# Kernel tuning notes

Measured on AMD Instinct MI355X. Metric: run time of the kernel, lower is better.

The kernel has to match this reference:

```python
import jax, jax.numpy as jnp
import numpy as np

NUM_ROUNDS = 64
D_HIDDEN = 256
B = 16384

# MD5 message schedule g(i)
_SCHED = np.array([i if i < 16 else ((5*i+1) % 16 if i < 32 else ((3*i+5) % 16 if i < 48 else (7*i) % 16)) for i in range(64)], dtype=np.int32)
# MD5 per-round shift amounts
_SHIFT = np.array([7,12,17,22]*4 + [5,9,14,20]*4 + [4,11,16,23]*4 + [6,10,15,21]*4, dtype=np.float32)
# round_info[i] = [i/64, shift[i]/25], shape (64, 2)
_ROUND_INFO = np.stack([np.arange(64, dtype=np.float32) / 64.0, _SHIFT / 25.0], axis=-1)


def setup_inputs() -> dict:
    key = jax.random.key(0)
    ks = jax.random.split(key, 8)
    return {
        "message_bytes": jax.random.uniform(ks[0], (B, 64), dtype=jnp.float32),
        "initial_state": jax.random.uniform(ks[1], (B, 16), dtype=jnp.float32),
        "W1": jax.random.normal(ks[2], (NUM_ROUNDS, 22, D_HIDDEN), dtype=jnp.float32) * (1.0 / np.sqrt(22.0)),
        "b1": jax.random.normal(ks[3], (NUM_ROUNDS, D_HIDDEN), dtype=jnp.float32) * 0.02,
        "W2": jax.random.normal(ks[4], (NUM_ROUNDS, D_HIDDEN, D_HIDDEN), dtype=jnp.float32) * (1.0 / np.sqrt(float(D_HIDDEN))),
        "b2": jax.random.normal(ks[5], (NUM_ROUNDS, D_HIDDEN), dtype=jnp.float32) * 0.02,
        "W3": jax.random.normal(ks[6], (NUM_ROUNDS, D_HIDDEN, 16), dtype=jnp.float32) * (1.0 / np.sqrt(float(D_HIDDEN))),
        "b3": jax.random.normal(ks[7], (NUM_ROUNDS, 16), dtype=jnp.float32) * 0.02,
    }


def reference(message_bytes, initial_state, W1, b1, W2, b2, W3, b3):
    Bsz = message_bytes.shape[0]
    msg_words = message_bytes.reshape(Bsz, 16, 4)
    # pre-gather the scheduled word per round: (64, B, 4)
    words = jnp.transpose(msg_words[:, jnp.asarray(_SCHED), :], (1, 0, 2))
    round_info = jnp.asarray(_ROUND_INFO)  # (64, 2)

    def step(state, xs):
        word, rinfo, w1, c1, w2, c2, w3, c3 = xs
        x = jnp.concatenate([state, word, jnp.broadcast_to(rinfo, (state.shape[0], 2))], axis=-1)  # (B, 22)
        h = jax.nn.gelu(x @ w1 + c1, approximate=False)
        h = jax.nn.gelu(h @ w2 + c2, approximate=False)
        return h @ w3 + c3, None

    final_state, _ = jax.lax.scan(step, initial_state, (words, round_info, W1, b1, W2, b2, W3, b3))
    return final_state
```

## Files before the change

kernel.cpp:

```cpp
#include <hip/hip_runtime.h>
#include <stdint.h>


using bf16x8   = __attribute__((ext_vector_type(8))) __bf16;
using floatx4  = __attribute__((ext_vector_type(4))) float;
using ushort4v = __attribute__((ext_vector_type(4))) unsigned short;

__constant__ int c_sched[64] = {
  0,1,2,3,4,5,6,7,8,9,10,11,12,13,14,15,
  1,6,11,0,5,10,15,4,9,14,3,8,13,2,7,12,
  5,8,11,14,1,4,7,10,13,0,3,6,9,12,15,2,
  0,7,14,5,12,3,10,1,8,15,6,13,4,11,2,9
};
__constant__ float c_shift[64] = {
  7,12,17,22,7,12,17,22,7,12,17,22,7,12,17,22,
  5,9,14,20,5,9,14,20,5,9,14,20,5,9,14,20,
  4,11,16,23,4,11,16,23,4,11,16,23,4,11,16,23,
  6,10,15,21,6,10,15,21,6,10,15,21,6,10,15,21
};

__device__ __forceinline__ unsigned short bfbits(__bf16 b) {
  union { __bf16 b; unsigned short u; } v; v.b = b; return v.u;
}
__device__ __forceinline__ float gelu_f(float x) {
  float ax = fabsf(x);
  float t  = __builtin_amdgcn_rcpf(__builtin_fmaf(0.33270222f, ax, 1.0f));
  float e  = __builtin_amdgcn_exp2f(x * x * -0.72134752f);
  float poly = t * __builtin_fmaf(t, __builtin_fmaf(t, 0.7478556f, -0.0958798f),
                                  0.3480242f);
  float er = __builtin_fmaf(-poly, e, 1.0f);
  er = copysignf(er, x);
  float hx = 0.5f * x;
  return __builtin_fmaf(hx, er, hx);
}
__device__ __forceinline__ floatx4 mfma16(bf16x8 a, bf16x8 b, floatx4 c) {
  return __builtin_amdgcn_mfma_f32_16x16x32_bf16(a, b, c, 0, 0, 0);
}
struct BfPair { unsigned short h, l; };
__device__ __forceinline__ BfPair split2(float s) {
  __bf16 hb = (__bf16)s;
  __bf16 lb = (__bf16)(s - (float)hb);
  BfPair p; p.h = bfbits(hb); p.l = bfbits(lb); return p;
}

#define N1G (64*16*64)
#define N2G (64*16*8*64)
#define N3G (64*8*64)

__global__ void pack_w(const float* __restrict__ W1,
                       const float* __restrict__ W2,
                       const float* __restrict__ W3,
                       unsigned short* __restrict__ P) {
  int gid = blockIdx.x * blockDim.x + threadIdx.x;
  if (gid >= N1G + N2G + N3G) return;
  unsigned short v[8];
  unsigned short* dst;
  if (gid < N1G) {
    int lane = gid & 63, t = (gid >> 6) & 15, r = gid >> 10;
    int qq = lane >> 4, mm = lane & 15;
    #pragma unroll
    for (int j = 0; j < 8; ++j) {
      int k = 8*qq + j;
      v[j] = (k < 22) ? bfbits((__bf16)W1[(r*22 + k)*256 + 16*t + mm]) : (unsigned short)0;
    }
    dst = P + (size_t)gid * 8;
  } else if (gid < N1G + N2G) {
    int g = gid - N1G;
    int lane = g & 63, c = (g >> 6) & 7, t = (g >> 9) & 15, r = g >> 13;
    int qq = lane >> 4, mm = lane & 15;
    #pragma unroll
    for (int j = 0; j < 8; ++j) {
      int k = 32*c + 8*qq + j;
      v[j] = bfbits((__bf16)W2[((size_t)r*256 + k)*256 + 16*t + mm]);
    }
    dst = P + (size_t)(N1G + g) * 8;
  } else {
    int g = gid - N1G - N2G;
    int lane = g & 63, c = (g >> 6) & 7, r = g >> 9;
    int qq = lane >> 4, mm = lane & 15;
    #pragma unroll
    for (int j = 0; j < 8; ++j) {
      int k = 32*c + 8*qq + j;
      v[j] = bfbits((__bf16)W3[(r*256 + k)*16 + mm]);
    }
    dst = P + (size_t)(N1G + N2G + g) * 8;
  }
  ushort4v lo = { v[0],v[1],v[2],v[3] }, hi = { v[4],v[5],v[6],v[7] };
  *(ushort4v*)dst = lo;
  *(ushort4v*)(dst + 4) = hi;
}

#define NG  2
#define SXW 36
#define SH 264
#define SM 66

__global__ __launch_bounds__(256, 2) void md5_main(
    const float* __restrict__ msg,
    const float* __restrict__ st0,
    const float* __restrict__ b1,
    const float* __restrict__ b2,
    const float* __restrict__ b3,
    const unsigned short* __restrict__ P,
    float* __restrict__ out)
{
  __shared__ unsigned short xh[4][NG][16][SXW], xl[4][NG][16][SXW];
  __shared__ unsigned short hA[NG][16][SH], hB[NG][16][SH];
  __shared__ unsigned short msgb[NG*16][SM], msgl[NG*16][SM];

  const int tid  = threadIdx.x;
  const int wv   = tid >> 6;
  const int lane = tid & 63;
  const int q    = lane >> 4;
  const int ln   = lane & 15;
  const int row0 = blockIdx.x * (NG*16);

  const unsigned short* P1 = P;
  const unsigned short* P2 = P + (size_t)N1G * 8;
  const unsigned short* P3 = P + (size_t)(N1G + N2G) * 8;

  for (int i = lane; i < NG*16*SXW; i += 64) {
    (&xh[wv][0][0][0])[i] = 0; (&xl[wv][0][0][0])[i] = 0;
  }
  {
    int idx = tid * 8, rr = idx >> 6, cc = idx & 63;
    floatx4 v0 = *(const floatx4*)(msg + (size_t)(row0 + rr)*64 + cc);
    floatx4 v1 = *(const floatx4*)(msg + (size_t)(row0 + rr)*64 + cc + 4);
    #pragma unroll
    for (int j = 0; j < 4; ++j) {
      BfPair p0 = split2(v0[j]);
      BfPair p1 = split2(v1[j]);
      msgb[rr][cc + j]     = p0.h;  msgl[rr][cc + j]     = p0.l;
      msgb[rr][cc + 4 + j] = p1.h;  msgl[rr][cc + 4 + j] = p1.l;
    }
  }
  #pragma unroll
  for (int g = 0; g < NG; ++g) {
    floatx4 v = *(const floatx4*)(st0 + (size_t)(row0 + g*16 + ln)*16 + 4*q);
    ushort4v h4, l4;
    #pragma unroll
    for (int e = 0; e < 4; ++e) { BfPair p = split2(v[e]); h4[e] = p.h; l4[e] = p.l; }
    *(ushort4v*)&xh[wv][g][ln][4*q] = h4;
    *(ushort4v*)&xl[wv][g][ln][4*q] = l4;
  }
  __syncthreads();
  if (lane < NG*16) {
    int g = lane >> 4, n = lane & 15, rrow = lane;
    int s = c_sched[0];
    BfPair i1p = split2(c_shift[0] / 25.0f);
    #pragma unroll
    for (int j = 0; j < 4; ++j) {
      xh[wv][g][n][16+j] = msgb[rrow][4*s+j];
      xl[wv][g][n][16+j] = msgl[rrow][4*s+j];
    }
    xh[wv][g][n][20] = 0;     xl[wv][g][n][20] = 0;
    xh[wv][g][n][21] = i1p.h; xl[wv][g][n][21] = i1p.l;
  }

  #pragma unroll 1
  for (int r = 0; r < 64; ++r) {
    floatx4 bb1[4];
    bf16x8  a1[4];
    const unsigned short* p1 = P1 + ((size_t)(r*16 + 4*wv)*64 + lane)*8;
    #pragma unroll
    for (int tt = 0; tt < 4; ++tt) {
      a1[tt]  = *(const bf16x8*)(p1 + (size_t)tt*512);
      bb1[tt] = *(const floatx4*)(b1 + r*256 + (4*wv + tt)*16 + 4*q);
    }
    bf16x8 bxh[NG], bxl[NG];
    #pragma unroll
    for (int g = 0; g < NG; ++g) {
      bxh[g] = *(const bf16x8*)&xh[wv][g][ln][8*q];
      bxl[g] = *(const bf16x8*)&xl[wv][g][ln][8*q];
    }
    #pragma unroll
    for (int tt = 0; tt < 4; ++tt) {
      int f0 = (4*wv + tt)*16 + 4*q;
      #pragma unroll
      for (int g = 0; g < NG; ++g) {
        floatx4 acc = bb1[tt];
        acc = mfma16(a1[tt], bxl[g], acc);
        acc = mfma16(a1[tt], bxh[g], acc);
        ushort4v h4;
        #pragma unroll
        for (int e = 0; e < 4; ++e) h4[e] = bfbits((__bf16)gelu_f(acc[e]));
        *(ushort4v*)&hA[g][ln][f0] = h4;
      }
    }
    __syncthreads();

    bf16x8 a3[8];
    {
      const unsigned short* p3 = P3 + ((size_t)(r*8)*64 + lane)*8;
      #pragma unroll
      for (int c = 0; c < 8; ++c) a3[c] = *(const bf16x8*)(p3 + (size_t)c*512);
    }
    floatx4 bb3 = *(const floatx4*)(b3 + r*16 + 4*q);
    floatx4 bb2[4];
    #pragma unroll
    for (int tt = 0; tt < 4; ++tt)
      bb2[tt] = *(const floatx4*)(b2 + r*256 + (4*wv + tt)*16 + 4*q);

    bf16x8 Bf[NG][8];
    #pragma unroll
    for (int g = 0; g < NG; ++g)
      #pragma unroll
      for (int c = 0; c < 8; ++c) Bf[g][c] = *(const bf16x8*)&hA[g][ln][32*c + 8*q];

    const unsigned short* p2 = P2 + ((size_t)((r*16 + 4*wv)*8)*64 + lane)*8;
    #pragma unroll
    for (int tt = 0; tt < 4; ++tt) {
      bf16x8 a2[8];
      #pragma unroll
      for (int c = 0; c < 8; ++c)
        a2[c] = *(const bf16x8*)(p2 + (size_t)(tt*8 + c)*512);
      int f0 = (4*wv + tt)*16 + 4*q;
      #pragma unroll
      for (int g = 0; g < NG; ++g) {
        floatx4 acc = bb2[tt];
        #pragma unroll
        for (int c = 0; c < 8; ++c) acc = mfma16(a2[c], Bf[g][c], acc);
        ushort4v h4;
        #pragma unroll
        for (int e = 0; e < 4; ++e) h4[e] = bfbits((__bf16)gelu_f(acc[e]));
        *(ushort4v*)&hB[g][ln][f0] = h4;
      }
    }
    __syncthreads();

    #pragma unroll
    for (int g = 0; g < NG; ++g) {
      floatx4 s = bb3;
      #pragma unroll
      for (int c = 0; c < 8; ++c) {
        bf16x8 bh = *(const bf16x8*)&hB[g][ln][32*c + 8*q];
        s = mfma16(a3[c], bh, s);
      }
      if (r == 63) {
        if (wv == 0)
          *(floatx4*)(out + (size_t)(row0 + g*16 + ln)*16 + 4*q) = s;
      } else {
        ushort4v h4, l4;
        #pragma unroll
        for (int e = 0; e < 4; ++e) { BfPair p = split2(s[e]); h4[e] = p.h; l4[e] = p.l; }
        *(ushort4v*)&xh[wv][g][ln][4*q] = h4;
        *(ushort4v*)&xl[wv][g][ln][4*q] = l4;
      }
    }
    if (lane < NG*16 && r < 63) {
      int g = lane >> 4, n = lane & 15, rrow = lane;
      int sc = c_sched[r+1];
      float i0 = (float)(r+1) * 0.015625f;
      BfPair i1p = split2(c_shift[r+1] / 25.0f);
      #pragma unroll
      for (int j = 0; j < 4; ++j) {
        xh[wv][g][n][16+j] = msgb[rrow][4*sc+j];
        xl[wv][g][n][16+j] = msgl[rrow][4*sc+j];
      }
      xh[wv][g][n][20] = bfbits((__bf16)i0); xl[wv][g][n][20] = 0;
      xh[wv][g][n][21] = i1p.h;              xl[wv][g][n][21] = i1p.l;
    }
  }
}

extern "C" void kernel_launch(void* const* d_in, const int* in_sizes, int n_in,
                              void* d_out, int out_size, void* d_ws, size_t ws_size,
                              hipStream_t stream) {
  const float* msg = (const float*)d_in[0];
  const float* st0 = (const float*)d_in[1];
  const float* W1  = (const float*)d_in[2];
  const float* b1  = (const float*)d_in[3];
  const float* W2  = (const float*)d_in[4];
  const float* b2  = (const float*)d_in[5];
  const float* W3  = (const float*)d_in[6];
  const float* b3  = (const float*)d_in[7];
  float* out = (float*)d_out;
  (void)in_sizes; (void)n_in; (void)out_size; (void)ws_size;

  unsigned short* P = (unsigned short*)d_ws;
  const int totalGroups = N1G + N2G + N3G;
  pack_w<<<(totalGroups + 255) / 256, 256, 0, stream>>>(W1, W2, W3, P);
  md5_main<<<512, 256, 0, stream>>>(msg, st0, b1, b2, b3, P, out);
}
```

Measured before the change: 466.4 us.

## Keep per-round state input fragment in registers via permuted W3 and lane shuffles

Removes the per-wave shared-memory xh/xl staging buffers for the 22-wide layer-1 input. W3 columns are permuted at pack time so each lane's layer-3 MFMA output lines up with the B-fragment layout of the next round's layer-1 MFMA. The fragment is then built in registers with xor-32 shuffles plus the message word and round info. This drops LDS writes and reads and the lane-restricted fixup each round, and with less LDS the occupancy hint rises from 2 to 3 blocks. The cost is more register pressure and the added shuffles.

```diff
diff --git a/kernel.cpp b/kernel.cpp
--- a/kernel.cpp
+++ b/kernel.cpp
@@ -22,6 +22,13 @@
 __device__ __forceinline__ unsigned short bfbits(__bf16 b) {
   union { __bf16 b; unsigned short u; } v; v.b = b; return v.u;
 }
+__device__ __forceinline__ float bf2f(unsigned short h) {
+  union { unsigned u; float f; } v; v.u = ((unsigned)h) << 16;
+  return v.f;
+}
+__device__ __forceinline__ int pack2(unsigned short lo16, unsigned short hi16) {
+  return (int)(((unsigned)hi16 << 16) | (unsigned)lo16);
+}
 __device__ __forceinline__ float gelu_f(float x) {
   float ax = fabsf(x);
   float t  = __builtin_amdgcn_rcpf(__builtin_fmaf(0.33270222f, ax, 1.0f));
@@ -36,11 +43,33 @@
 __device__ __forceinline__ floatx4 mfma16(bf16x8 a, bf16x8 b, floatx4 c) {
   return __builtin_amdgcn_mfma_f32_16x16x32_bf16(a, b, c, 0, 0, 0);
 }
-struct BfPair { unsigned short h, l; };
-__device__ __forceinline__ BfPair split2(float s) {
-  __bf16 hb = (__bf16)s;
-  __bf16 lb = (__bf16)(s - (float)hb);
-  BfPair p; p.h = bfbits(hb); p.l = bfbits(lb); return p;
+
+__device__ __forceinline__ void build_frag(int* fh, int* fl, floatx4 s,
+                                           int w01, int w23, int wl01, int wl23,
+                                           int i01h, int i01l,
+                                           bool isQ2, bool isQ3) {
+  unsigned short h0 = bfbits((__bf16)s[0]);
+  unsigned short h1 = bfbits((__bf16)s[1]);
+  unsigned short h2 = bfbits((__bf16)s[2]);
+  unsigned short h3 = bfbits((__bf16)s[3]);
+  unsigned short l0 = bfbits((__bf16)(s[0] - bf2f(h0)));
+  unsigned short l1 = bfbits((__bf16)(s[1] - bf2f(h1)));
+  unsigned short l2 = bfbits((__bf16)(s[2] - bf2f(h2)));
+  unsigned short l3 = bfbits((__bf16)(s[3] - bf2f(h3)));
+  int oh0 = pack2(h0, h1), oh1 = pack2(h2, h3);
+  int ol0 = pack2(l0, l1), ol1 = pack2(l2, l3);
+  int th0 = __shfl_xor(oh0, 32);
+  int th1 = __shfl_xor(oh1, 32);
+  int tl0 = __shfl_xor(ol0, 32);
+  int tl1 = __shfl_xor(ol1, 32);
+  fh[0] = isQ3 ? 0 : (isQ2 ? w01  : oh0);
+  fh[1] = isQ3 ? 0 : (isQ2 ? w23  : oh1);
+  fh[2] = isQ3 ? 0 : (isQ2 ? i01h : th0);
+  fh[3] = isQ3 ? 0 : (isQ2 ? 0    : th1);
+  fl[0] = isQ3 ? 0 : (isQ2 ? wl01 : ol0);
+  fl[1] = isQ3 ? 0 : (isQ2 ? wl23 : ol1);
+  fl[2] = isQ3 ? 0 : (isQ2 ? i01l : tl0);
+  fl[3] = isQ3 ? 0 : (isQ2 ? 0    : tl1);
 }
 
 #define N1G (64*16*64)
@@ -78,10 +107,11 @@
     int g = gid - N1G - N2G;
     int lane = g & 63, c = (g >> 6) & 7, r = g >> 9;
     int qq = lane >> 4, mm = lane & 15;
+    int fm = 8*((mm >> 2) & 1) + 4*(mm >> 3) + (mm & 3);
     #pragma unroll
     for (int j = 0; j < 8; ++j) {
       int k = 32*c + 8*qq + j;
-      v[j] = bfbits((__bf16)W3[(r*256 + k)*16 + mm]);
+      v[j] = bfbits((__bf16)W3[(r*256 + k)*16 + fm]);
     }
     dst = P + (size_t)(N1G + N2G + g) * 8;
   }
@@ -90,12 +120,11 @@
   *(ushort4v*)(dst + 4) = hi;
 }
 
-#define NG  2
-#define SXW 36
+#define NG 2
 #define SH 264
-#define SM 66
-
-__global__ __launch_bounds__(256, 2) void md5_main(
+#define SM 68
+
+__global__ __launch_bounds__(256, 3) void md5_main(
     const float* __restrict__ msg,
     const float* __restrict__ st0,
     const float* __restrict__ b1,
@@ -104,7 +133,6 @@
     const unsigned short* __restrict__ P,
     float* __restrict__ out)
 {
-  __shared__ unsigned short xh[4][NG][16][SXW], xl[4][NG][16][SXW];
   __shared__ unsigned short hA[NG][16][SH], hB[NG][16][SH];
   __shared__ unsigned short msgb[NG*16][SM], msgl[NG*16][SM];
 
@@ -114,47 +142,45 @@
   const int q    = lane >> 4;
   const int ln   = lane & 15;
   const int row0 = blockIdx.x * (NG*16);
+  const int oPerm = 8*(q & 1) + 4*(q >> 1);
+  const bool isQ2 = (q == 2), isQ3 = (q == 3);
 
   const unsigned short* P1 = P;
   const unsigned short* P2 = P + (size_t)N1G * 8;
   const unsigned short* P3 = P + (size_t)(N1G + N2G) * 8;
 
-  for (int i = lane; i < NG*16*SXW; i += 64) {
-    (&xh[wv][0][0][0])[i] = 0; (&xl[wv][0][0][0])[i] = 0;
-  }
   {
     int idx = tid * 8, rr = idx >> 6, cc = idx & 63;
     floatx4 v0 = *(const floatx4*)(msg + (size_t)(row0 + rr)*64 + cc);
     floatx4 v1 = *(const floatx4*)(msg + (size_t)(row0 + rr)*64 + cc + 4);
     #pragma unroll
     for (int j = 0; j < 4; ++j) {
-      BfPair p0 = split2(v0[j]);
-      BfPair p1 = split2(v1[j]);
-      msgb[rr][cc + j]     = p0.h;  msgl[rr][cc + j]     = p0.l;
-      msgb[rr][cc + 4 + j] = p1.h;  msgl[rr][cc + 4 + j] = p1.l;
-    }
-  }
-  #pragma unroll
-  for (int g = 0; g < NG; ++g) {
-    floatx4 v = *(const floatx4*)(st0 + (size_t)(row0 + g*16 + ln)*16 + 4*q);
-    ushort4v h4, l4;
-    #pragma unroll
-    for (int e = 0; e < 4; ++e) { BfPair p = split2(v[e]); h4[e] = p.h; l4[e] = p.l; }
-    *(ushort4v*)&xh[wv][g][ln][4*q] = h4;
-    *(ushort4v*)&xl[wv][g][ln][4*q] = l4;
+      unsigned short h0 = bfbits((__bf16)v0[j]);
+      unsigned short h1 = bfbits((__bf16)v1[j]);
+      msgb[rr][cc + j]     = h0;
+      msgb[rr][cc + 4 + j] = h1;
+      msgl[rr][cc + j]     = bfbits((__bf16)(v0[j] - bf2f(h0)));
+      msgl[rr][cc + 4 + j] = bfbits((__bf16)(v1[j] - bf2f(h1)));
+    }
   }
   __syncthreads();
-  if (lane < NG*16) {
-    int g = lane >> 4, n = lane & 15, rrow = lane;
-    int s = c_sched[0];
-    BfPair i1p = split2(c_shift[0] / 25.0f);
-    #pragma unroll
-    for (int j = 0; j < 4; ++j) {
-      xh[wv][g][n][16+j] = msgb[rrow][4*s+j];
-      xl[wv][g][n][16+j] = msgl[rrow][4*s+j];
-    }
-    xh[wv][g][n][20] = 0;     xl[wv][g][n][20] = 0;
-    xh[wv][g][n][21] = i1p.h; xl[wv][g][n][21] = i1p.l;
+
+  int fxh[NG][4], fxl[NG][4];
+
+  {
+    int sc = c_sched[0];
+    float i1 = c_shift[0] * 0.04f;
+    unsigned short i1h = bfbits((__bf16)i1);
+    unsigned short i1l = bfbits((__bf16)(i1 - bf2f(i1h)));
+    int i01h = pack2(0, i1h);
+    int i01l = pack2(0, i1l);
+    #pragma unroll
+    for (int g = 0; g < NG; ++g) {
+      floatx4 s = *(const floatx4*)(st0 + (size_t)(row0 + g*16 + ln)*16 + oPerm);
+      int2 wh = *(const int2*)&msgb[g*16 + ln][4*sc];
+      int2 wl = *(const int2*)&msgl[g*16 + ln][4*sc];
+      build_frag(fxh[g], fxl[g], s, wh.x, wh.y, wl.x, wl.y, i01h, i01l, isQ2, isQ3);
+    }
   }
 
   #pragma unroll 1
@@ -167,11 +193,13 @@
       a1[tt]  = *(const bf16x8*)(p1 + (size_t)tt*512);
       bb1[tt] = *(const floatx4*)(b1 + r*256 + (4*wv + tt)*16 + 4*q);
     }
-    bf16x8 bxh[NG], bxl[NG];
+    bf16x8 xh_[NG], xl_[NG];
     #pragma unroll
     for (int g = 0; g < NG; ++g) {
-      bxh[g] = *(const bf16x8*)&xh[wv][g][ln][8*q];
-      bxl[g] = *(const bf16x8*)&xl[wv][g][ln][8*q];
+      union { int i[4]; bf16x8 v; } uh, ul;
+      #pragma unroll
+      for (int k = 0; k < 4; ++k) { uh.i[k] = fxh[g][k]; ul.i[k] = fxl[g][k]; }
+      xh_[g] = uh.v; xl_[g] = ul.v;
     }
     #pragma unroll
     for (int tt = 0; tt < 4; ++tt) {
@@ -179,8 +207,8 @@
       #pragma unroll
       for (int g = 0; g < NG; ++g) {
         floatx4 acc = bb1[tt];
-        acc = mfma16(a1[tt], bxl[g], acc);
-        acc = mfma16(a1[tt], bxh[g], acc);
+        acc = mfma16(a1[tt], xl_[g], acc);
+        acc = mfma16(a1[tt], xh_[g], acc);
         ushort4v h4;
         #pragma unroll
         for (int e = 0; e < 4; ++e) h4[e] = bfbits((__bf16)gelu_f(acc[e]));
@@ -195,11 +223,28 @@
       #pragma unroll
       for (int c = 0; c < 8; ++c) a3[c] = *(const bf16x8*)(p3 + (size_t)c*512);
     }
-    floatx4 bb3 = *(const floatx4*)(b3 + r*16 + 4*q);
+    floatx4 bb3 = *(const floatx4*)(b3 + r*16 + oPerm);
     floatx4 bb2[4];
     #pragma unroll
     for (int tt = 0; tt < 4; ++tt)
       bb2[tt] = *(const floatx4*)(b2 + r*256 + (4*wv + tt)*16 + 4*q);
+
+    int2 wh[NG], wl[NG];
+    int i01h = 0, i01l = 0;
+    if (r < 63) {
+      int sc = c_sched[r+1];
+      float i0 = (float)(r+1) * 0.015625f;
+      float i1 = c_shift[r+1] * 0.04f;
+      unsigned short i1h = bfbits((__bf16)i1);
+      unsigned short i1l = bfbits((__bf16)(i1 - bf2f(i1h)));
+      i01h = pack2(bfbits((__bf16)i0), i1h);
+      i01l = pack2(0, i1l);
+      #pragma unroll
+      for (int g = 0; g < NG; ++g) {
+        wh[g] = *(const int2*)&msgb[g*16 + ln][4*sc];
+        wl[g] = *(const int2*)&msgl[g*16 + ln][4*sc];
+      }
+    }
 
     bf16x8 Bf[NG][8];
     #pragma unroll
@@ -238,27 +283,11 @@
       }
       if (r == 63) {
         if (wv == 0)
-          *(floatx4*)(out + (size_t)(row0 + g*16 + ln)*16 + 4*q) = s;
+          *(floatx4*)(out + (size_t)(row0 + g*16 + ln)*16 + oPerm) = s;
       } else {
-        ushort4v h4, l4;
-        #pragma unroll
-        for (int e = 0; e < 4; ++e) { BfPair p = split2(s[e]); h4[e] = p.h; l4[e] = p.l; }
-        *(ushort4v*)&xh[wv][g][ln][4*q] = h4;
-        *(ushort4v*)&xl[wv][g][ln][4*q] = l4;
-      }
-    }
-    if (lane < NG*16 && r < 63) {
-      int g = lane >> 4, n = lane & 15, rrow = lane;
-      int sc = c_sched[r+1];
-      float i0 = (float)(r+1) * 0.015625f;
-      BfPair i1p = split2(c_shift[r+1] / 25.0f);
-      #pragma unroll
-      for (int j = 0; j < 4; ++j) {
-        xh[wv][g][n][16+j] = msgb[rrow][4*sc+j];
-        xl[wv][g][n][16+j] = msgl[rrow][4*sc+j];
-      }
-      xh[wv][g][n][20] = bfbits((__bf16)i0); xl[wv][g][n][20] = 0;
-      xh[wv][g][n][21] = i1p.h;              xl[wv][g][n][21] = i1p.l;
+        build_frag(fxh[g], fxl[g], s, wh[g].x, wh[g].y, wl[g].x, wl[g].y,
+                   i01h, i01l, isQ2, isQ3);
+      }
     }
   }
 }
```

After: 682.6 us. 1.46x slower.
